# Performance work log

Hardware: AMD Instinct MI355X
Metric: run time of the kernel (lower is better)

## Reference

```python
import jax, jax.numpy as jnp
import numpy as np

NGRAM_N = 4

def ngram_repeat_mask(toks, n):
    # toks: [B, S] int32. Mark positions j..j+n-1 for every ngram starting at
    # j (j in range(S-n)) that already appeared at an earlier start position.
    B, S = toks.shape
    P = S - n  # number of ngram start positions, matching range(len(x)-n)
    win = jnp.arange(P)[:, None] + jnp.arange(n)[None, :]  # [P, n]
    G = toks[:, win]                                        # [B, P, n]
    eq = (G[:, :, None, :] == G[:, None, :, :]).all(-1)     # [B, P, P]
    prev = jnp.tril(jnp.ones((P, P), dtype=bool), k=-1)     # j' < j
    repeated = (eq & prev[None]).any(-1)                    # [B, P]
    # dilate forward over the ngram window: mask[j:j+n] = 1 if repeated[j]
    shifted = jnp.stack([jnp.pad(repeated, ((0, 0), (k, S - P - k)))
                         for k in range(n)], axis=0)        # [n, B, S]
    return shifted.any(0).astype(jnp.float32)               # [B, S]

def setup_inputs() -> dict:
    key = jax.random.key(0)
    B, V, S = 8, 32000, 512
    pred = jax.random.normal(key, (B, V, S), dtype=jnp.float32)
    return {"pred": pred}

def reference(pred):
    # pred: [B, V, S] logits
    B = pred.shape[0]
    pred_toks = jnp.argmax(pred, axis=1)                    # [B, S] int
    pred_lprobs_full = jax.nn.log_softmax(pred, axis=1)     # [B, V, S]
    # gather log-prob of the argmax token at each position -> [B, S]
    pred_lprobs = jnp.take_along_axis(pred_lprobs_full, pred_toks[:, None, :], axis=1)[:, 0, :]
    one_minus_probs = jnp.clip(1.0 - jnp.exp(pred_lprobs), 1e-20, None)
    mask = ngram_repeat_mask(pred_toks, NGRAM_N)            # [B, S] float
    loss = (-jnp.log(one_minus_probs) * mask).sum() / B
    return loss
```

## Files before the change

### kernel.cpp

```cpp
#include <hip/hip_runtime.h>
#include <math.h>

#define BB 8
#define VV 32000
#define SS 512
#define NCHUNK 64
#define CHUNK (VV / NCHUNK)
#define NCOL (BB * SS)
#define NGRAM 4
#define PP (SS - NGRAM)

__global__ __launch_bounds__(256) void colstats_kernel(const float* __restrict__ pred,
                                                       float* __restrict__ pmax,
                                                       float* __restrict__ psum,
                                                       int* __restrict__ pidx) {
    const int bid = blockIdx.x;
    const int b   = bid >> 6;
    const int c   = bid & (NCHUNK - 1);
    const int tid = threadIdx.x;
    const int vo  = tid >> 7;
    const int s   = (tid & 127) << 2;
    const int v0  = c * CHUNK;

    float m0 = -INFINITY, m1 = -INFINITY, m2 = -INFINITY, m3 = -INFINITY;
    float a0 = 0.f, a1 = 0.f, a2 = 0.f, a3 = 0.f;
    int   i0 = 0, i1 = 0, i2 = 0, i3 = 0;

    const float L2E = 1.4426950408889634f;
    const float* ptr = pred + ((size_t)(b * VV + v0 + vo)) * SS + s;
#pragma unroll 4
    for (int v = v0 + vo; v < v0 + CHUNK; v += 2) {
        const float4 x = *(const float4*)ptr;
        ptr += 2 * SS;
        a0 += exp2f(x.x * L2E);
        a1 += exp2f(x.y * L2E);
        a2 += exp2f(x.z * L2E);
        a3 += exp2f(x.w * L2E);
        if (x.x > m0) { m0 = x.x; i0 = v; }
        if (x.y > m1) { m1 = x.y; i1 = v; }
        if (x.z > m2) { m2 = x.z; i2 = v; }
        if (x.w > m3) { m3 = x.w; i3 = v; }
    }

    __shared__ float smax[256][4];
    __shared__ float ssum[256][4];
    __shared__ int   sidx[256][4];
    smax[tid][0] = m0; smax[tid][1] = m1; smax[tid][2] = m2; smax[tid][3] = m3;
    ssum[tid][0] = a0; ssum[tid][1] = a1; ssum[tid][2] = a2; ssum[tid][3] = a3;
    sidx[tid][0] = i0; sidx[tid][1] = i1; sidx[tid][2] = i2; sidx[tid][3] = i3;
    __syncthreads();

    if (tid < 128) {
        const int o = tid + 128;
        float m[4]  = {smax[tid][0], smax[tid][1], smax[tid][2], smax[tid][3]};
        float a[4]  = {ssum[tid][0], ssum[tid][1], ssum[tid][2], ssum[tid][3]};
        int   ix[4] = {sidx[tid][0], sidx[tid][1], sidx[tid][2], sidx[tid][3]};
#pragma unroll
        for (int j = 0; j < 4; ++j) {
            const float om = smax[o][j];
            const int   oi = sidx[o][j];
            a[j] += ssum[o][j];
            if (om > m[j] || (om == m[j] && oi < ix[j])) { m[j] = om; ix[j] = oi; }
        }
        const size_t ob = (size_t)c * NCOL + (size_t)b * SS + (size_t)s;
#pragma unroll
        for (int j = 0; j < 4; ++j) {
            pmax[ob + j] = m[j];
            psum[ob + j] = a[j];
            pidx[ob + j] = ix[j];
        }
    }
}

__global__ __launch_bounds__(256) void finalize_kernel(const float* __restrict__ pmax,
                                                       const float* __restrict__ psum,
                                                       const int* __restrict__ pidx,
                                                       int* __restrict__ toks,
                                                       float* __restrict__ pen) {
    const int col = blockIdx.x * 256 + threadIdx.x;
    float m = -INFINITY;
    float sum = 0.f;
    int   idx = 0;
    for (int c = 0; c < NCHUNK; ++c) {
        const int off = c * NCOL + col;
        const float cm = pmax[off];
        const int   ci = pidx[off];
        sum += psum[off];
        if (cm > m || (cm == m && ci < idx)) { m = cm; idx = ci; }
    }
    const float lprob = m - logf(sum);
    const float p = expf(lprob);
    float om = 1.0f - p;
    if (om < 1e-20f) om = 1e-20f;
    pen[col]  = -logf(om);
    toks[col] = idx;
}

__global__ void zero_kernel(float* out) { out[0] = 0.0f; }

__global__ __launch_bounds__(256) void mask_loss_kernel(const int* __restrict__ toks,
                                                        const float* __restrict__ pen,
                                                        float* __restrict__ out) {
    const int b   = blockIdx.x;
    const int tid = threadIdx.x;
    __shared__ int tk[SS];
    __shared__ int rep[SS];
    for (int i = tid; i < SS; i += 256) { tk[i] = toks[b * SS + i]; rep[i] = 0; }
    __syncthreads();

    for (int i = tid; i < PP; i += 256) {
        const int c0 = tk[i], c1 = tk[i + 1], c2 = tk[i + 2], c3 = tk[i + 3];
        int r = 0;
        for (int j = 0; j < i; ++j) {
            if (tk[j] == c0 && tk[j + 1] == c1 && tk[j + 2] == c2 && tk[j + 3] == c3) {
                r = 1; break;
            }
        }
        rep[i] = r;
    }
    __syncthreads();

    float local = 0.f;
    for (int s = tid; s < SS; s += 256) {
        int msk = 0;
#pragma unroll
        for (int k = 0; k < NGRAM; ++k) {
            const int i = s - k;
            if (i >= 0 && i < PP && rep[i]) msk = 1;
        }
        if (msk) local += pen[b * SS + s];
    }

    for (int off = 32; off > 0; off >>= 1) local += __shfl_down(local, off, 64);
    __shared__ float wsum[4];
    const int lane = tid & 63, wid = tid >> 6;
    if (lane == 0) wsum[wid] = local;
    __syncthreads();
    if (tid == 0) {
        float t = wsum[0] + wsum[1] + wsum[2] + wsum[3];
        atomicAdd(out, t * (1.0f / (float)BB));
    }
}

extern "C" void kernel_launch(void* const* d_in, const int* in_sizes, int n_in,
                              void* d_out, int out_size, void* d_ws, size_t ws_size,
                              hipStream_t stream) {
    const float* pred = (const float*)d_in[0];
    float* out = (float*)d_out;
    char* ws = (char*)d_ws;

    const size_t partN = (size_t)NCHUNK * NCOL;
    float* pmax = (float*)ws;
    float* psum = (float*)(ws + partN * 4);
    int*   pidx = (int*)  (ws + partN * 8);
    int*   toks = (int*)  (ws + partN * 12);
    float* pen  = (float*)(ws + partN * 12 + NCOL * 4);

    colstats_kernel<<<BB * NCHUNK, 256, 0, stream>>>(pred, pmax, psum, pidx);
    finalize_kernel<<<NCOL / 256, 256, 0, stream>>>(pmax, psum, pidx, toks, pen);
    zero_kernel<<<1, 1, 0, stream>>>(out);
    mask_loss_kernel<<<BB, 256, 0, stream>>>(toks, pen, out);
}
```

Measured before the change: 765.2 us.

## Use more vocab chunks, split finalize reduction across threads, drop zero kernel

Vocab chunks grow from 64 to 125 of 256 rows each, so colstats launches 1000 blocks instead of 512, which fills the GPU better. The finalize kernel now has four threads per column, each reducing about 32 chunks, and combines them through shared memory, so it no longer runs one serial loop per column over all chunks. Zeroing the output is folded into finalize, which removes one kernel launch. The cost is more partial-result traffic through the workspace and extra shared-memory reduction steps.

```diff
diff --git a/kernel.cpp b/kernel.cpp
--- a/kernel.cpp
+++ b/kernel.cpp
@@ -4,8 +4,8 @@
 #define BB 8
 #define VV 32000
 #define SS 512
-#define NCHUNK 64
-#define CHUNK (VV / NCHUNK)
+#define NCHUNK 125
+#define CHUNK 256
 #define NCOL (BB * SS)
 #define NGRAM 4
 #define PP (SS - NGRAM)
@@ -15,8 +15,8 @@
                                                        float* __restrict__ psum,
                                                        int* __restrict__ pidx) {
     const int bid = blockIdx.x;
-    const int b   = bid >> 6;
-    const int c   = bid & (NCHUNK - 1);
+    const int b   = bid / NCHUNK;
+    const int c   = bid - b * NCHUNK;
     const int tid = threadIdx.x;
     const int vo  = tid >> 7;
     const int s   = (tid & 127) << 2;
@@ -28,8 +28,9 @@
 
     const float L2E = 1.4426950408889634f;
     const float* ptr = pred + ((size_t)(b * VV + v0 + vo)) * SS + s;
-#pragma unroll 4
-    for (int v = v0 + vo; v < v0 + CHUNK; v += 2) {
+    int v = v0 + vo;
+#pragma unroll 8
+    for (int k = 0; k < CHUNK / 2; ++k) {
         const float4 x = *(const float4*)ptr;
         ptr += 2 * SS;
         a0 += exp2f(x.x * L2E);
@@ -40,6 +41,7 @@
         if (x.y > m1) { m1 = x.y; i1 = v; }
         if (x.z > m2) { m2 = x.z; i2 = v; }
         if (x.w > m3) { m3 = x.w; i3 = v; }
+        v += 2;
     }
 
     __shared__ float smax[256][4];
@@ -76,27 +78,48 @@
                                                        const float* __restrict__ psum,
                                                        const int* __restrict__ pidx,
                                                        int* __restrict__ toks,
-                                                       float* __restrict__ pen) {
-    const int col = blockIdx.x * 256 + threadIdx.x;
-    float m = -INFINITY;
-    float sum = 0.f;
-    int   idx = 0;
-    for (int c = 0; c < NCHUNK; ++c) {
+                                                       float* __restrict__ pen,
+                                                       float* __restrict__ out) {
+    const int tid  = threadIdx.x;
+    const int col  = blockIdx.x * 64 + (tid >> 2);
+    const int part = tid & 3;
+
+    if (blockIdx.x == 0 && tid == 0) out[0] = 0.0f;
+
+    const int cbeg = part * 32;
+    int cend = cbeg + 32; if (cend > NCHUNK) cend = NCHUNK;
+
+    float m = -INFINITY, sum = 0.f;
+    int   idx = 0x7fffffff;
+    for (int c = cbeg; c < cend; ++c) {
         const int off = c * NCOL + col;
         const float cm = pmax[off];
         const int   ci = pidx[off];
         sum += psum[off];
         if (cm > m || (cm == m && ci < idx)) { m = cm; idx = ci; }
     }
-    const float lprob = m - logf(sum);
-    const float p = expf(lprob);
-    float om = 1.0f - p;
-    if (om < 1e-20f) om = 1e-20f;
-    pen[col]  = -logf(om);
-    toks[col] = idx;
+
+    __shared__ float sm[256], ss[256];
+    __shared__ int   si[256];
+    sm[tid] = m; ss[tid] = sum; si[tid] = idx;
+    __syncthreads();
+
+    if (part == 0) {
+#pragma unroll
+        for (int j = 1; j < 4; ++j) {
+            const float om = sm[tid + j];
+            const int   oi = si[tid + j];
+            sum += ss[tid + j];
+            if (om > m || (om == m && oi < idx)) { m = om; idx = oi; }
+        }
+        const float lprob = m - logf(sum);
+        const float p = expf(lprob);
+        float om1 = 1.0f - p;
+        if (om1 < 1e-20f) om1 = 1e-20f;
+        pen[col]  = -logf(om1);
+        toks[col] = idx;
+    }
 }
-
-__global__ void zero_kernel(float* out) { out[0] = 0.0f; }
 
 __global__ __launch_bounds__(256) void mask_loss_kernel(const int* __restrict__ toks,
                                                         const float* __restrict__ pen,
@@ -157,7 +180,6 @@
     float* pen  = (float*)(ws + partN * 12 + NCOL * 4);
 
     colstats_kernel<<<BB * NCHUNK, 256, 0, stream>>>(pred, pmax, psum, pidx);
-    finalize_kernel<<<NCOL / 256, 256, 0, stream>>>(pmax, psum, pidx, toks, pen);
-    zero_kernel<<<1, 1, 0, stream>>>(out);
+    finalize_kernel<<<NCOL / 64, 256, 0, stream>>>(pmax, psum, pidx, toks, pen, out);
     mask_loss_kernel<<<BB, 256, 0, stream>>>(toks, pen, out);
 }
```

Measured after the change: 755.9 us. No clear change (-1.2%).
